# Optimization experiments

Measured on AMD Instinct MI355X. Metric: run time of the kernel, lower is better.

The kernel has to match this reference:

```python
import jax, jax.numpy as jnp
import numpy as np

B, D_IN, H, T_EMB = 16384, 256, 512, 16


def _lin_params(key, out_dim, in_dim, bias):
    k1, k2 = jax.random.split(key)
    s = 1.0 / np.sqrt(in_dim)
    W = jax.random.uniform(k1, (out_dim, in_dim), jnp.float32, -s, s)
    b = jax.random.uniform(k2, (out_dim,), jnp.float32, -s, s) if bias else None
    return W, b


def setup_inputs() -> dict:
    key = jax.random.key(0)
    ks = jax.random.split(key, 20)
    x = jax.random.normal(ks[0], (B, D_IN), jnp.float32)
    h = jax.random.normal(ks[1], (B, H), jnp.float32)
    c_prev = jax.random.normal(ks[2], (B, H), jnp.float32)
    delt = jax.random.uniform(ks[3], (B, T_EMB), jnp.float32)

    W_ix, b_ix = _lin_params(ks[4], H, D_IN, True)
    W_ih, _ = _lin_params(ks[5], H, H, False)
    W_ic, _ = _lin_params(ks[6], H, H, False)
    W_fx, b_fx = _lin_params(ks[7], H, D_IN, True)
    W_fh, _ = _lin_params(ks[8], H, H, False)
    W_fc, _ = _lin_params(ks[9], H, H, False)
    W_tx, b_tx = _lin_params(ks[10], H, D_IN, True)
    W_tt, _ = _lin_params(ks[11], H, T_EMB, False)
    W_cx, b_cx = _lin_params(ks[12], H, D_IN, True)
    W_ch, _ = _lin_params(ks[13], H, H, False)
    W_ox, b_ox = _lin_params(ks[14], H, D_IN, True)
    W_oh, _ = _lin_params(ks[15], H, H, False)
    W_oc, _ = _lin_params(ks[16], H, H, False)
    W_ot, _ = _lin_params(ks[17], H, T_EMB, False)

    return dict(x=x, h=h, c_prev=c_prev, delt=delt,
                W_ix=W_ix, b_ix=b_ix, W_ih=W_ih, W_ic=W_ic,
                W_fx=W_fx, b_fx=b_fx, W_fh=W_fh, W_fc=W_fc,
                W_tx=W_tx, b_tx=b_tx, W_tt=W_tt,
                W_cx=W_cx, b_cx=b_cx, W_ch=W_ch,
                W_ox=W_ox, b_ox=b_ox, W_oh=W_oh, W_oc=W_oc, W_ot=W_ot)


def reference(x, h, c_prev, delt,
              W_ix, b_ix, W_ih, W_ic,
              W_fx, b_fx, W_fh, W_fc,
              W_tx, b_tx, W_tt,
              W_cx, b_cx, W_ch,
              W_ox, b_ox, W_oh, W_oc, W_ot):
    sig, tanh = jax.nn.sigmoid, jnp.tanh
    # input gate
    i = sig(x @ W_ix.T + b_ix + h @ W_ih.T + c_prev @ W_ic.T)
    # forget gate
    f = sig(x @ W_fx.T + b_fx + h @ W_fh.T + c_prev @ W_fc.T)
    # time gate: note inner sigmoid on the time-delta projection
    T = sig(x @ W_tx.T + b_tx + sig(delt @ W_tt.T))
    # candidate cell and new cell state
    k = tanh(x @ W_cx.T + b_cx + h @ W_ch.T)
    c_next = i * T * k + f * c_prev
    # output gate
    o = sig(x @ W_ox.T + b_ox + delt @ W_ot.T + h @ W_oh.T + c_prev @ W_oc.T)
    h_next = o * tanh(c_next)
    return (h_next, c_next, T)
```

## Files before the change

### kernel.cpp

```cpp
#include <hip/hip_runtime.h>
#include <cstdint>

#define B_SZ   16384
#define H_SZ   512
#define DIN    256
#define TEMB   16
#define KP     1344
#define KPB    1344
#define BH     8388608L
#define SLOT   24576
#define TSLOT  20480
#define GSTR   688128

typedef __attribute__((ext_vector_type(4))) float f32x4;
typedef __attribute__((ext_vector_type(4))) int   i32x4;

typedef const __attribute__((address_space(1))) unsigned int gu32_t;
typedef __attribute__((address_space(3)))       unsigned int lu32_t;

__device__ __forceinline__ void gld16(const void* g, void* l) {
  __builtin_amdgcn_global_load_lds((gu32_t*)(uintptr_t)g,
                                   (lu32_t*)(unsigned int)(uintptr_t)l, 16, 0, 0);
}

__device__ __forceinline__ float sigm(float v)  { return 1.0f / (1.0f + __expf(-v)); }
__device__ __forceinline__ float tanhx(float v) { return 2.0f / (1.0f + __expf(-2.0f * v)) - 1.0f; }

__device__ __forceinline__ signed char q8(float v, float inv) {
  int q = __float2int_rn(v * inv);
  q = (q > 127) ? 127 : (q < -127 ? -127 : q);
  return (signed char)q;
}

__global__ void prep_a8_kernel(const float* __restrict__ x, const float* __restrict__ h,
                               const float* __restrict__ c, const float* __restrict__ dl,
                               signed char* __restrict__ Ap, float* __restrict__ sa) {
  __shared__ float row[KP];
  __shared__ float red[256];
  const int m   = blockIdx.x;
  const int tid = threadIdx.x;
  float lmax = 0.f;
  for (int i = tid; i < KP / 4; i += 256) {
    const int k4 = i * 4;
    float4 v = make_float4(0.f, 0.f, 0.f, 0.f);
    if (k4 < 256)       v = *(const float4*)(x  + (size_t)m * DIN  + k4);
    else if (k4 < 768)  v = *(const float4*)(h  + (size_t)m * H_SZ + (k4 - 256));
    else if (k4 < 1280) v = *(const float4*)(c  + (size_t)m * H_SZ + (k4 - 768));
    else if (k4 < 1296) v = *(const float4*)(dl + (size_t)m * TEMB + (k4 - 1280));
    *(float4*)(row + k4) = v;
    lmax = fmaxf(lmax, fmaxf(fmaxf(fabsf(v.x), fabsf(v.y)), fmaxf(fabsf(v.z), fabsf(v.w))));
  }
  red[tid] = lmax;
  __syncthreads();
  for (int s = 128; s > 0; s >>= 1) {
    if (tid < s) red[tid] = fmaxf(red[tid], red[tid + s]);
    __syncthreads();
  }
  const float smax = fmaxf(red[0], 1e-20f);
  const float inv  = 127.0f / smax;
  if (tid == 0) sa[m] = smax * (1.0f / 127.0f);
  for (int i = tid; i < KP / 4; i += 256) {
    const int k4 = i * 4;
    char4 o;
    o.x = q8(row[k4],     inv); o.y = q8(row[k4 + 1], inv);
    o.z = q8(row[k4 + 2], inv); o.w = q8(row[k4 + 3], inv);
    *(char4*)(Ap + (size_t)m * KPB + k4) = o;
  }
}

__global__ void prep_w8_kernel(const float* __restrict__ Wix, const float* __restrict__ Wih, const float* __restrict__ Wic,
                               const float* __restrict__ Wfx, const float* __restrict__ Wfh, const float* __restrict__ Wfc,
                               const float* __restrict__ Wtx, const float* __restrict__ Wtt,
                               const float* __restrict__ Wcx, const float* __restrict__ Wch,
                               const float* __restrict__ Wox, const float* __restrict__ Woh,
                               const float* __restrict__ Woc, const float* __restrict__ Wot,
                               signed char* __restrict__ Wp, float* __restrict__ sw) {
  __shared__ float row[KP];
  __shared__ float red[256];
  const int R   = blockIdx.x;
  const int g   = R >> 9;
  const int n   = R & 511;
  const int tid = threadIdx.x;
  float lmax = 0.f;
  for (int i = tid; i < KP / 4; i += 256) {
    const int k4 = i * 4;
    const float* src = nullptr; long o = 0;
    if (g == 0) {
      if (k4 < 256)       { src = Wix; o = (long)n * 256 + k4; }
      else if (k4 < 768)  { src = Wih; o = (long)n * 512 + (k4 - 256); }
      else if (k4 < 1280) { src = Wic; o = (long)n * 512 + (k4 - 768); }
    } else if (g == 1) {
      if (k4 < 256)       { src = Wfx; o = (long)n * 256 + k4; }
      else if (k4 < 768)  { src = Wfh; o = (long)n * 512 + (k4 - 256); }
      else if (k4 < 1280) { src = Wfc; o = (long)n * 512 + (k4 - 768); }
    } else if (g == 2) {
      if (k4 < 256)       { src = Wtx; o = (long)n * 256 + k4; }
    } else if (g == 3) {
      if (k4 < 256)       { src = Wcx; o = (long)n * 256 + k4; }
      else if (k4 < 768)  { src = Wch; o = (long)n * 512 + (k4 - 256); }
    } else if (g == 4) {
      if (k4 < 256)       { src = Wox; o = (long)n * 256 + k4; }
      else if (k4 < 768)  { src = Woh; o = (long)n * 512 + (k4 - 256); }
      else if (k4 < 1280) { src = Woc; o = (long)n * 512 + (k4 - 768); }
      else if (k4 < 1296) { src = Wot; o = (long)n * 16 + (k4 - 1280); }
    } else {
      if (k4 >= 1280 && k4 < 1296) { src = Wtt; o = (long)n * 16 + (k4 - 1280); }
    }
    float4 v = make_float4(0.f, 0.f, 0.f, 0.f);
    if (src) v = *(const float4*)(src + o);
    *(float4*)(row + k4) = v;
    lmax = fmaxf(lmax, fmaxf(fmaxf(fabsf(v.x), fabsf(v.y)), fmaxf(fabsf(v.z), fabsf(v.w))));
  }
  red[tid] = lmax;
  __syncthreads();
  for (int s = 128; s > 0; s >>= 1) {
    if (tid < s) red[tid] = fmaxf(red[tid], red[tid + s]);
    __syncthreads();
  }
  const float smax = fmaxf(red[0], 1e-20f);
  const float inv  = 127.0f / smax;
  if (tid == 0) sw[R] = smax * (1.0f / 127.0f);
  for (int i = tid; i < KP / 4; i += 256) {
    const int k4 = i * 4;
    char4 o;
    o.x = q8(row[k4],     inv); o.y = q8(row[k4 + 1], inv);
    o.z = q8(row[k4 + 2], inv); o.w = q8(row[k4 + 3], inv);
    *(char4*)(Wp + (size_t)R * KPB + k4) = o;
  }
}


template<unsigned SMASK>
__device__ __forceinline__ void stage(char* lds, int sb, int ht,
                                      const char* sAb, const char* sWb, int wid) {
  const unsigned kb = (unsigned)ht * 64u;
  gld16(sAb + kb,              lds + sb + wid * 2048);
  gld16(sAb + kb + 16u * KPB,  lds + sb + wid * 2048 + 1024);
  const int r = wid >> 1, c = wid & 1;
  if (SMASK & (1u << r)) {
    const int g = r + (r >> 1);
    gld16(sWb + (unsigned)g * GSTR + (unsigned)c * (16u * KPB) + kb,
          lds + sb + 16384 + r * 2048 + c * 1024);
  }
}

template<unsigned CM>
__device__ __forceinline__ void comp(const char* lds, int sb, int aro, int wro,
                                     i32x4 acc[4][4]) {
  const char* base = lds + sb;
  i32x4 a[4];
#pragma unroll
  for (int i = 0; i < 4; ++i)
    a[i] = *(const i32x4*)(base + aro + i * 1024);
  __builtin_amdgcn_s_setprio(1);
#pragma unroll
  for (int r = 0; r < 4; ++r) {
    if (CM & (1u << r)) {
      i32x4 b = *(const i32x4*)(base + 16384 + r * 2048 + wro);
#pragma unroll
      for (int i = 0; i < 4; ++i)
        acc[r][i] = __builtin_amdgcn_mfma_i32_16x16x64_i8(a[i], b, acc[r][i], 0, 0, 0);
    }
  }
  __builtin_amdgcn_s_setprio(0);
}

template<unsigned CM, unsigned SM, bool ST>
__device__ __forceinline__ void phase(char* lds, int h, const char* sAb, const char* sWb,
                                      int wid, int aro, int wro, i32x4 acc[4][4]) {
  if (ST) stage<SM>(lds, ((h + 1) & 1) * SLOT, h + 1, sAb, sWb, wid);
  comp<CM>(lds, (h & 1) * SLOT, aro, wro, acc);
  __syncthreads();
}

__global__ __launch_bounds__(512, 4) void lstm_main(
    const signed char* __restrict__ Ap, const signed char* __restrict__ Wp,
    const float* __restrict__ sa, const float* __restrict__ sw,
    const float* __restrict__ c_prev,
    const float* __restrict__ b_ix, const float* __restrict__ b_fx,
    const float* __restrict__ b_cx, const float* __restrict__ b_ox,
    float* __restrict__ out)
{
  __shared__ __align__(16) char lds[2 * SLOT];

  const int tid  = threadIdx.x;
  const int lane = tid & 63;
  const int wid  = tid >> 6;

  const int bid = blockIdx.x;
  const int xcd = bid & 7;
  const int idx = bid >> 3;
  const int cb  = (xcd << 1) | (idx & 1);
  const int rb  = idx >> 1;
  const unsigned brow = (unsigned)rb * 256u;
  const int bcol = cb * 32;

  const int wr  = (wid >> 1) * 64;
  const int wcg = (wid & 1) * 16;
  const int lrow = lane & 15;
  const int kgrp = lane >> 4;

  i32x4 acc[4][4];
  {
    i32x4 z = {0, 0, 0, 0};
#pragma unroll
    for (int g = 0; g < 4; ++g)
#pragma unroll
      for (int i = 0; i < 4; ++i) acc[g][i] = z;
  }

  const int sread = ((kgrp + (lrow >> 1)) & 3) << 4;
  const int aro = (wr + lrow) * 64 + sread;
  const int wro = (wcg + lrow) * 64 + sread;

  const int l4 = lane >> 2;
  const int kslot = (((lane & 3) - ((lane >> 3) & 3)) & 3) << 4;
  const char* sAb = (const char*)Ap + (size_t)(brow + wid * 32 + l4) * KPB + kslot;
  const char* sWb = (const char*)Wp + (size_t)(bcol + l4) * KPB + kslot;

  stage<0xF>(lds, 0, 0, sAb, sWb, wid);
  __syncthreads();

#pragma unroll 1
  for (int h = 0; h < 11; ++h)
    phase<0xF, 0xF, true>(lds, h, sAb, sWb, wid, aro, wro, acc);
  phase<0xF, 0xB, true>(lds, 11, sAb, sWb, wid, aro, wro, acc);
#pragma unroll 1
  for (int h = 12; h < 19; ++h)
    phase<0xB, 0xB, true>(lds, h, sAb, sWb, wid, aro, wro, acc);
  phase<0xB, 0x8, true>(lds, 19, sAb, sWb, wid, aro, wro, acc);
  comp<0x8>(lds, (20 & 1) * SLOT, aro, wro, acc);

  const float* Tvp = out + 2 * BH;
  const int n = bcol + wcg + lrow;
  const float bi = b_ix[n], bff = b_fx[n], bc = b_cx[n], bo = b_ox[n];
  const float s0 = sw[0 * 512 + n], s1 = sw[1 * 512 + n];
  const float s3 = sw[3 * 512 + n], s4 = sw[4 * 512 + n];
  const int rbase = kgrp * 4;
#pragma unroll
  for (int i = 0; i < 4; ++i) {
    const int m0 = (int)brow + wr + 16 * i + rbase;
    const float4 sa4 = *(const float4*)(sa + m0);
#pragma unroll
    for (int r = 0; r < 4; ++r) {
      const long m   = m0 + r;
      const long off = m * H_SZ + n;
      const float sr = (r == 0) ? sa4.x : (r == 1) ? sa4.y : (r == 2) ? sa4.z : sa4.w;
      const float iv = sigm((float)acc[0][i][r] * sr * s0 + bi);
      const float fv = sigm((float)acc[1][i][r] * sr * s1 + bff);
      const float kv = tanhx((float)acc[2][i][r] * sr * s3 + bc);
      const float ov = sigm((float)acc[3][i][r] * sr * s4 + bo);
      const float Tv = Tvp[off];
      const float cp = c_prev[off];
      const float cn = iv * Tv * kv + fv * cp;
      out[off]      = ov * tanhx(cn);
      out[BH + off] = cn;
    }
  }
}

template<unsigned SMASK>
__device__ __forceinline__ void stage_t(char* lds, int sb, int ht,
                                        const char* sAb, const char* sWb, int wid) {
  const unsigned kb = (unsigned)ht * 64u;
  gld16(sAb + kb,              lds + sb + wid * 2048);
  gld16(sAb + kb + 16u * KPB,  lds + sb + wid * 2048 + 1024);
  if (wid < 4) {
    const int r = wid >> 1, c = wid & 1;
    if (SMASK & (1u << r)) {
      const int g = (r == 0) ? 2 : 5;
      gld16(sWb + (unsigned)g * GSTR + (unsigned)c * (16u * KPB) + kb,
            lds + sb + 16384 + r * 2048 + c * 1024);
    }
  }
}

template<unsigned CM>
__device__ __forceinline__ void comp_t(const char* lds, int sb, int aro, int wro,
                                       i32x4 acc[2][4]) {
  const char* base = lds + sb;
  i32x4 a[4];
#pragma unroll
  for (int i = 0; i < 4; ++i)
    a[i] = *(const i32x4*)(base + aro + i * 1024);
#pragma unroll
  for (int r = 0; r < 2; ++r) {
    if (CM & (1u << r)) {
      i32x4 b = *(const i32x4*)(base + 16384 + r * 2048 + wro);
#pragma unroll
      for (int i = 0; i < 4; ++i)
        acc[r][i] = __builtin_amdgcn_mfma_i32_16x16x64_i8(a[i], b, acc[r][i], 0, 0, 0);
    }
  }
}

__global__ __launch_bounds__(512, 4) void tgate_kernel(
    const signed char* __restrict__ Ap, const signed char* __restrict__ Wp,
    const float* __restrict__ sa, const float* __restrict__ sw,
    const float* __restrict__ b_tx, float* __restrict__ out)
{
  __shared__ __align__(16) char lds[2 * TSLOT];

  const int tid  = threadIdx.x;
  const int lane = tid & 63;
  const int wid  = tid >> 6;

  const int bid = blockIdx.x;
  const int xcd = bid & 7;
  const int idx = bid >> 3;
  const int cb  = (xcd << 1) | (idx & 1);
  const int rb  = idx >> 1;
  const unsigned brow = (unsigned)rb * 256u;
  const int bcol = cb * 32;

  const int wr  = (wid >> 1) * 64;
  const int wcg = (wid & 1) * 16;
  const int lrow = lane & 15;
  const int kgrp = lane >> 4;

  i32x4 acc[2][4];
  {
    i32x4 z = {0, 0, 0, 0};
#pragma unroll
    for (int g = 0; g < 2; ++g)
#pragma unroll
      for (int i = 0; i < 4; ++i) acc[g][i] = z;
  }

  const int sread = ((kgrp + (lrow >> 1)) & 3) << 4;
  const int aro = (wr + lrow) * 64 + sread;
  const int wro = (wcg + lrow) * 64 + sread;

  const int l4 = lane >> 2;
  const int kslot = (((lane & 3) - ((lane >> 3) & 3)) & 3) << 4;
  const char* sAb = (const char*)Ap + (size_t)(brow + wid * 32 + l4) * KPB + kslot;
  const char* sWb = (const char*)Wp + (size_t)(bcol + l4) * KPB + kslot;

  stage_t<0x1>(lds, 0, 0, sAb, sWb, wid);
  __syncthreads();
  stage_t<0x1>(lds, TSLOT, 1, sAb, sWb, wid);
  comp_t<0x1>(lds, 0, aro, wro, acc);
  __syncthreads();
  stage_t<0x1>(lds, 0, 2, sAb, sWb, wid);
  comp_t<0x1>(lds, TSLOT, aro, wro, acc);
  __syncthreads();
  stage_t<0x1>(lds, TSLOT, 3, sAb, sWb, wid);
  comp_t<0x1>(lds, 0, aro, wro, acc);
  __syncthreads();
  stage_t<0x2>(lds, 0, 20, sAb, sWb, wid);
  comp_t<0x1>(lds, TSLOT, aro, wro, acc);
  __syncthreads();
  comp_t<0x2>(lds, 0, aro, wro, acc);

  const int n = bcol + wcg + lrow;
  const float bt = b_tx[n];
  const float s2 = sw[2 * 512 + n], s5 = sw[5 * 512 + n];
  const int rbase = kgrp * 4;
#pragma unroll
  for (int i = 0; i < 4; ++i) {
    const int m0 = (int)brow + wr + 16 * i + rbase;
    const float4 sa4 = *(const float4*)(sa + m0);
#pragma unroll
    for (int r = 0; r < 4; ++r) {
      const long off = (long)(m0 + r) * H_SZ + n;
      const float sr = (r == 0) ? sa4.x : (r == 1) ? sa4.y : (r == 2) ? sa4.z : sa4.w;
      const float inner = sigm((float)acc[1][i][r] * sr * s5);
      out[2 * BH + off] = sigm((float)acc[0][i][r] * sr * s2 + bt + inner);
    }
  }
}

extern "C" void kernel_launch(void* const* d_in, const int* in_sizes, int n_in,
                              void* d_out, int out_size, void* d_ws, size_t ws_size,
                              hipStream_t stream) {
  const float* x      = (const float*)d_in[0];
  const float* h      = (const float*)d_in[1];
  const float* c_prev = (const float*)d_in[2];
  const float* dl     = (const float*)d_in[3];
  const float* W_ix = (const float*)d_in[4];
  const float* b_ix = (const float*)d_in[5];
  const float* W_ih = (const float*)d_in[6];
  const float* W_ic = (const float*)d_in[7];
  const float* W_fx = (const float*)d_in[8];
  const float* b_fx = (const float*)d_in[9];
  const float* W_fh = (const float*)d_in[10];
  const float* W_fc = (const float*)d_in[11];
  const float* W_tx = (const float*)d_in[12];
  const float* b_tx = (const float*)d_in[13];
  const float* W_tt = (const float*)d_in[14];
  const float* W_cx = (const float*)d_in[15];
  const float* b_cx = (const float*)d_in[16];
  const float* W_ch = (const float*)d_in[17];
  const float* W_ox = (const float*)d_in[18];
  const float* b_ox = (const float*)d_in[19];
  const float* W_oh = (const float*)d_in[20];
  const float* W_oc = (const float*)d_in[21];
  const float* W_ot = (const float*)d_in[22];

  signed char* Ap8 = (signed char*)d_ws;
  signed char* Wp8 = (signed char*)d_ws + (size_t)B_SZ * KPB;
  float* sa = (float*)((char*)d_ws + (size_t)B_SZ * KPB + 6L * H_SZ * KPB);
  float* sw = sa + B_SZ;

  prep_a8_kernel<<<B_SZ, 256, 0, stream>>>(x, h, c_prev, dl, Ap8, sa);
  prep_w8_kernel<<<6 * H_SZ, 256, 0, stream>>>(
      W_ix, W_ih, W_ic, W_fx, W_fh, W_fc, W_tx, W_tt, W_cx, W_ch,
      W_ox, W_oh, W_oc, W_ot, Wp8, sw);

  tgate_kernel<<<1024, 512, 0, stream>>>(Ap8, Wp8, sa, sw, b_tx, (float*)d_out);

  lstm_main<<<1024, 512, 0, stream>>>(Ap8, Wp8, sa, sw, c_prev,
                                      b_ix, b_fx, b_cx, b_ox,
                                      (float*)d_out);
}
```

Baseline: 130.3 us.

## Triple-buffer main GEMM LDS pipeline and use wave-per-row activation quantization

The main int8 MFMA loop moves from double to triple LDS buffering. Loads are issued two stages ahead, with explicit vmcnt waits and raw s_barrier calls replacing __syncthreads. The staging mask is removed, so W tiles are always loaded even when some gate groups go unused. Separately, the activation quantization kernel now gives each wave one row, keeping values in registers and reducing the row max with shuffles instead of an LDS tree with many barriers. The costs are more LDS per block, which may lower occupancy, plus some redundant W loads in the later phases.

```diff
diff --git a/kernel.cpp b/kernel.cpp
--- a/kernel.cpp
+++ b/kernel.cpp
@@ -35,36 +35,37 @@
 __global__ void prep_a8_kernel(const float* __restrict__ x, const float* __restrict__ h,
                                const float* __restrict__ c, const float* __restrict__ dl,
                                signed char* __restrict__ Ap, float* __restrict__ sa) {
-  __shared__ float row[KP];
-  __shared__ float red[256];
-  const int m   = blockIdx.x;
-  const int tid = threadIdx.x;
+  const int tid  = threadIdx.x;
+  const int lane = tid & 63;
+  const int m    = blockIdx.x * 4 + (tid >> 6);
+  float4 v[6];
   float lmax = 0.f;
-  for (int i = tid; i < KP / 4; i += 256) {
-    const int k4 = i * 4;
-    float4 v = make_float4(0.f, 0.f, 0.f, 0.f);
-    if (k4 < 256)       v = *(const float4*)(x  + (size_t)m * DIN  + k4);
-    else if (k4 < 768)  v = *(const float4*)(h  + (size_t)m * H_SZ + (k4 - 256));
-    else if (k4 < 1280) v = *(const float4*)(c  + (size_t)m * H_SZ + (k4 - 768));
-    else if (k4 < 1296) v = *(const float4*)(dl + (size_t)m * TEMB + (k4 - 1280));
-    *(float4*)(row + k4) = v;
-    lmax = fmaxf(lmax, fmaxf(fmaxf(fabsf(v.x), fabsf(v.y)), fmaxf(fabsf(v.z), fabsf(v.w))));
-  }
-  red[tid] = lmax;
-  __syncthreads();
-  for (int s = 128; s > 0; s >>= 1) {
-    if (tid < s) red[tid] = fmaxf(red[tid], red[tid + s]);
-    __syncthreads();
-  }
-  const float smax = fmaxf(red[0], 1e-20f);
+#pragma unroll
+  for (int i = 0; i < 6; ++i) {
+    const int k4 = (i * 64 + lane) * 4;
+    float4 t = make_float4(0.f, 0.f, 0.f, 0.f);
+    if (k4 < 256)       t = *(const float4*)(x  + (size_t)m * DIN  + k4);
+    else if (k4 < 768)  t = *(const float4*)(h  + (size_t)m * H_SZ + (k4 - 256));
+    else if (k4 < 1280) t = *(const float4*)(c  + (size_t)m * H_SZ + (k4 - 768));
+    else if (k4 < 1296) t = *(const float4*)(dl + (size_t)m * TEMB + (k4 - 1280));
+    v[i] = t;
+    lmax = fmaxf(lmax, fmaxf(fmaxf(fabsf(t.x), fabsf(t.y)), fmaxf(fabsf(t.z), fabsf(t.w))));
+  }
+#pragma unroll
+  for (int s = 1; s < 64; s <<= 1)
+    lmax = fmaxf(lmax, __shfl_xor(lmax, s));
+  const float smax = fmaxf(lmax, 1e-20f);
   const float inv  = 127.0f / smax;
-  if (tid == 0) sa[m] = smax * (1.0f / 127.0f);
-  for (int i = tid; i < KP / 4; i += 256) {
-    const int k4 = i * 4;
-    char4 o;
-    o.x = q8(row[k4],     inv); o.y = q8(row[k4 + 1], inv);
-    o.z = q8(row[k4 + 2], inv); o.w = q8(row[k4 + 3], inv);
-    *(char4*)(Ap + (size_t)m * KPB + k4) = o;
+  if (lane == 0) sa[m] = smax * (1.0f / 127.0f);
+#pragma unroll
+  for (int i = 0; i < 6; ++i) {
+    const int k4 = (i * 64 + lane) * 4;
+    if (k4 < KP) {
+      char4 o;
+      o.x = q8(v[i].x, inv); o.y = q8(v[i].y, inv);
+      o.z = q8(v[i].z, inv); o.w = q8(v[i].w, inv);
+      *(char4*)(Ap + (size_t)m * KPB + k4) = o;
+    }
   }
 }
 
@@ -130,47 +131,46 @@
 }
 
 
-template<unsigned SMASK>
 __device__ __forceinline__ void stage(char* lds, int sb, int ht,
                                       const char* sAb, const char* sWb, int wid) {
   const unsigned kb = (unsigned)ht * 64u;
   gld16(sAb + kb,              lds + sb + wid * 2048);
   gld16(sAb + kb + 16u * KPB,  lds + sb + wid * 2048 + 1024);
   const int r = wid >> 1, c = wid & 1;
-  if (SMASK & (1u << r)) {
-    const int g = r + (r >> 1);
-    gld16(sWb + (unsigned)g * GSTR + (unsigned)c * (16u * KPB) + kb,
-          lds + sb + 16384 + r * 2048 + c * 1024);
-  }
-}
-
-template<unsigned CM>
-__device__ __forceinline__ void comp(const char* lds, int sb, int aro, int wro,
-                                     i32x4 acc[4][4]) {
-  const char* base = lds + sb;
+  const int g = r + (r >> 1);
+  gld16(sWb + (unsigned)g * GSTR + (unsigned)c * (16u * KPB) + kb,
+        lds + sb + 16384 + r * 2048 + c * 1024);
+}
+
+template<unsigned CM, int NW, bool ST>
+__device__ __forceinline__ void phase(char* lds, int rs, int ws, int ht,
+    const char* sAb, const char* sWb, int wid, int aro, int wro, i32x4 acc[4][4]) {
+  asm volatile("s_waitcnt vmcnt(%0)" :: "i"(NW) : "memory");
+  __builtin_amdgcn_s_barrier();
+  __builtin_amdgcn_sched_barrier(0);
+  const char* base = lds + rs;
   i32x4 a[4];
 #pragma unroll
   for (int i = 0; i < 4; ++i)
     a[i] = *(const i32x4*)(base + aro + i * 1024);
+  i32x4 b[4];
+#pragma unroll
+  for (int r = 0; r < 4; ++r)
+    if (CM & (1u << r))
+      b[r] = *(const i32x4*)(base + 16384 + r * 2048 + wro);
+  if (ST) stage(lds, ws, ht, sAb, sWb, wid);
+  asm volatile("s_waitcnt lgkmcnt(0)" ::: "memory");
+  __builtin_amdgcn_sched_barrier(0);
   __builtin_amdgcn_s_setprio(1);
 #pragma unroll
   for (int r = 0; r < 4; ++r) {
     if (CM & (1u << r)) {
-      i32x4 b = *(const i32x4*)(base + 16384 + r * 2048 + wro);
 #pragma unroll
       for (int i = 0; i < 4; ++i)
-        acc[r][i] = __builtin_amdgcn_mfma_i32_16x16x64_i8(a[i], b, acc[r][i], 0, 0, 0);
+        acc[r][i] = __builtin_amdgcn_mfma_i32_16x16x64_i8(a[i], b[r], acc[r][i], 0, 0, 0);
     }
   }
   __builtin_amdgcn_s_setprio(0);
-}
-
-template<unsigned CM, unsigned SM, bool ST>
-__device__ __forceinline__ void phase(char* lds, int h, const char* sAb, const char* sWb,
-                                      int wid, int aro, int wro, i32x4 acc[4][4]) {
-  if (ST) stage<SM>(lds, ((h + 1) & 1) * SLOT, h + 1, sAb, sWb, wid);
-  comp<CM>(lds, (h & 1) * SLOT, aro, wro, acc);
-  __syncthreads();
 }
 
 __global__ __launch_bounds__(512, 4) void lstm_main(
@@ -181,7 +181,7 @@
     const float* __restrict__ b_cx, const float* __restrict__ b_ox,
     float* __restrict__ out)
 {
-  __shared__ __align__(16) char lds[2 * SLOT];
+  __shared__ __align__(16) char lds[3 * SLOT];
 
   const int tid  = threadIdx.x;
   const int lane = tid & 63;
@@ -218,18 +218,24 @@
   const char* sAb = (const char*)Ap + (size_t)(brow + wid * 32 + l4) * KPB + kslot;
   const char* sWb = (const char*)Wp + (size_t)(bcol + l4) * KPB + kslot;
 
-  stage<0xF>(lds, 0, 0, sAb, sWb, wid);
-  __syncthreads();
+  stage(lds, 0,    0, sAb, sWb, wid);
+  stage(lds, SLOT, 1, sAb, sWb, wid);
+
+  int rs = 0;
+#define PH(CMv, NWv, STv, HT) do {                                             \
+    int ws = (rs >= SLOT) ? rs - SLOT : rs + 2 * SLOT;                         \
+    phase<CMv, NWv, STv>(lds, rs, ws, HT, sAb, sWb, wid, aro, wro, acc);       \
+    rs = (rs == 2 * SLOT) ? 0 : rs + SLOT;                                     \
+  } while (0)
 
 #pragma unroll 1
-  for (int h = 0; h < 11; ++h)
-    phase<0xF, 0xF, true>(lds, h, sAb, sWb, wid, aro, wro, acc);
-  phase<0xF, 0xB, true>(lds, 11, sAb, sWb, wid, aro, wro, acc);
+  for (int h = 0; h < 11; ++h) PH(0xF, 3, true, h + 2);
+  PH(0xF, 3, true, 13);
 #pragma unroll 1
-  for (int h = 12; h < 19; ++h)
-    phase<0xB, 0xB, true>(lds, h, sAb, sWb, wid, aro, wro, acc);
-  phase<0xB, 0x8, true>(lds, 19, sAb, sWb, wid, aro, wro, acc);
-  comp<0x8>(lds, (20 & 1) * SLOT, aro, wro, acc);
+  for (int h = 12; h < 19; ++h) PH(0xB, 3, true, h + 2);
+  PH(0xB, 3, false, 0);
+  PH(0x8, 0, false, 0);
+#undef PH
 
   const float* Tvp = out + 2 * BH;
   const int n = bcol + wcg + lrow;
@@ -402,7 +408,7 @@
   float* sa = (float*)((char*)d_ws + (size_t)B_SZ * KPB + 6L * H_SZ * KPB);
   float* sw = sa + B_SZ;
 
-  prep_a8_kernel<<<B_SZ, 256, 0, stream>>>(x, h, c_prev, dl, Ap8, sa);
+  prep_a8_kernel<<<B_SZ / 4, 256, 0, stream>>>(x, h, c_prev, dl, Ap8, sa);
   prep_w8_kernel<<<6 * H_SZ, 256, 0, stream>>>(
       W_ix, W_ih, W_ic, W_fx, W_fh, W_fc, W_tx, W_tt, W_cx, W_ch,
       W_ox, W_oh, W_oc, W_ot, Wp8, sw);
```

New measurement: 115.7 us. 1.13x faster.
